# Optimization experiments

Measured on AMD Instinct MI355X. Metric: run time of the kernel, lower is better.

The kernel has to match this reference:

```python
import jax, jax.numpy as jnp
import numpy as np

# dims: batch, time, measurements, heads, value-unit, channel C = H*VU
B, T, N = 16, 256, 128
H, VU = 8, 8
C = H * VU          # 64
TU, MU = 32, 32     # temporal / spatial head dims
L = 4               # encoder layers
FE = 4              # feed-forward expansion
NEG = -1e9


def setup_inputs() -> dict:
    key = jax.random.key(0)
    ks = jax.random.split(key, 20)
    def rn(k, shape, scale=0.02):
        return jax.random.normal(k, shape, jnp.float32) * scale
    return dict(
        values=jax.random.normal(ks[0], (B, T, N), jnp.float32),
        masks=(jax.random.uniform(ks[1], (B, T, N)) < 0.85).astype(jnp.float32),
        is_train=jnp.ones((B,), jnp.float32),
        conv1_w=rn(ks[2], (C,)), conv1_b=rn(ks[3], (C,)),
        conv2_w=rn(ks[4], (C,)), conv2_b=rn(ks[5], ()),
        ln1_g=jnp.ones((L, C)), ln1_b=jnp.zeros((L, C)),
        ln2_g=jnp.ones((L, C)), ln2_b=jnp.zeros((L, C)),
        Wv_s=rn(ks[6], (L, C, C)),
        Wk_s=rn(ks[7], (L, T * C, H * MU)),
        Wq_s=rn(ks[8], (L, T * C, H * MU)),
        Wv_t=rn(ks[9], (L, C, C)),
        Wk_t=rn(ks[10], (L, N * C, H * TU)),
        Wq_t=rn(ks[11], (L, N * C, H * TU)),
        Wr=rn(ks[12], (L, 2 * C, C)), br=jnp.zeros((L, C)),
        W1=rn(ks[13], (L, C, FE * C)), b1=jnp.zeros((L, FE * C)),
        W2=rn(ks[14], (L, FE * C, C)), b2=jnp.zeros((L, C)),
    )


def layer_norm(x, g, b):
    mu = x.mean(-1, keepdims=True)
    var = ((x - mu) ** 2).mean(-1, keepdims=True)
    return (x - mu) * jax.lax.rsqrt(var + 1e-5) * g + b


def attn_core(x, Wv, Wk, Wq, hd):
    # x: [B, A, E, C]; attend over A, the extra axis E is flattened into K/Q inputs
    B_, A, E, C_ = x.shape
    v = (x @ Wv).reshape(B_, A, E, H, VU)
    flat = x.reshape(B_, A, E * C_)
    q = (flat @ Wq).reshape(B_, A, H, hd)
    k = (flat @ Wk).reshape(B_, A, H, hd)
    energy = jnp.einsum('bqhd,bkhd->bqkh', q, k)            # [B, A, A, H]
    eye = jnp.eye(A, dtype=x.dtype)[None, :, :, None]
    energy = energy * (1.0 - eye) + eye * NEG               # exclude self (imputation mask)
    attn = jax.nn.softmax(energy / jnp.sqrt(jnp.asarray(hd, x.dtype)), axis=2)
    vflat = jnp.transpose(v, (0, 1, 3, 2, 4)).reshape(B_, A, H, E * VU)
    out = jnp.einsum('bqkh,bkhd->bqhd', attn, vflat)        # [B, A, H, E*VU]
    out = out.reshape(B_, A, H, E, VU).transpose(0, 1, 3, 2, 4).reshape(B_, A, E, C_)
    return out


def reference(values, masks, is_train, conv1_w, conv1_b, conv2_w, conv2_b,
              ln1_g, ln1_b, ln2_g, ln2_b, Wv_s, Wk_s, Wq_s, Wv_t, Wk_t, Wq_t,
              Wr, br, W1, b1, W2, b2):
    # conv1 is a 1x1 conv 1->C: per-element affine lift
    x = values[..., None] * conv1_w + conv1_b               # [B, T, N, C]
    for i in range(L):
        xn = layer_norm(x, ln1_g[i], ln1_b[i])
        sp = attn_core(jnp.swapaxes(xn, 1, 2), Wv_s[i], Wk_s[i], Wq_s[i], MU)  # spatial: attend over N
        sp = jnp.swapaxes(sp, 1, 2)
        tp = attn_core(xn, Wv_t[i], Wk_t[i], Wq_t[i], TU)                      # temporal: attend over T
        x0 = jnp.concatenate([sp, tp], axis=-1)             # [B, T, N, 2C]
        x1 = x0 @ Wr[i] + br[i] + x
        h = jax.nn.relu(layer_norm(x1, ln2_g[i], ln2_b[i]) @ W1[i] + b1[i])
        x = h @ W2[i] + b2[i] + x1
    out = x @ conv2_w + conv2_b                              # conv2 1x1 C->1: [B, T, N]
    per = (masks * (out - values) ** 2).reshape(B, -1).sum(-1) / masks.reshape(B, -1).sum(-1)
    loss = jnp.sum(per * is_train) / (jnp.sum(is_train) + 1e-5)
    return out, loss
```

## Files before the change

kernel.cpp:

```cpp
#include <hip/hip_runtime.h>

typedef unsigned short u16;
typedef unsigned int u32;
typedef __attribute__((ext_vector_type(8))) short short8;
typedef __attribute__((ext_vector_type(4))) float f32x4;

#define NEGSC (-1.7677669529663689e8f)
#define INVS  (0.17677669529663687f)

__device__ __forceinline__ u16 f2bf(float f) {
  union { float f; u32 u; } x{f};
  u32 r = x.u + 0x7fffu + ((x.u >> 16) & 1u);
  return (u16)(r >> 16);
}

__global__ __launch_bounds__(256) void k_lift(const float* __restrict__ values,
    const float* __restrict__ w, const float* __restrict__ b, float* __restrict__ x) {
  int i = blockIdx.x * 256 + threadIdx.x;
  int c = i & 63;
  int r = i >> 6;
  x[i] = values[r] * w[c] + b[c];
}

__global__ __launch_bounds__(256) void k_lnb(const float* __restrict__ in, u16* __restrict__ out,
    const float* __restrict__ g, const float* __restrict__ b) {
  int row = blockIdx.x * 4 + (threadIdx.x >> 6);
  int c = threadIdx.x & 63;
  float v = in[(size_t)row * 64 + c];
  float s = v;
  #pragma unroll
  for (int o = 32; o > 0; o >>= 1) s += __shfl_xor(s, o, 64);
  float mu = s * (1.f / 64.f);
  float d = v - mu;
  float q = d * d;
  #pragma unroll
  for (int o = 32; o > 0; o >>= 1) q += __shfl_xor(q, o, 64);
  out[(size_t)row * 64 + c] = f2bf(d * rsqrtf(q * (1.f / 64.f) + 1e-5f) * g[c] + b[c]);
}

__global__ __launch_bounds__(256) void k_trb(const int4* __restrict__ in, int4* __restrict__ out) {
  int idx = blockIdx.x * 256 + threadIdx.x;
  int c8 = idx & 7;
  int r = idx >> 3;
  int t = r & 255;
  int bn = r >> 8;
  int n = bn & 127;
  int b = bn >> 7;
  out[idx] = in[(((((b << 8) + t) << 7) + n) << 3) + c8];
}

__global__ __launch_bounds__(256) void k_wcast(const float* __restrict__ in, u16* __restrict__ out,
    int K, int N) {
  __shared__ float tile[32][33];
  int k0 = blockIdx.x * 32, n0 = blockIdx.y * 32;
  int tid = threadIdx.x;
  int kr = tid >> 3, nc = (tid & 7) * 4;
  float4 v = *(const float4*)(in + (size_t)(k0 + kr) * N + n0 + nc);
  tile[kr][nc + 0] = v.x; tile[kr][nc + 1] = v.y;
  tile[kr][nc + 2] = v.z; tile[kr][nc + 3] = v.w;
  __syncthreads();
  int nr = tid >> 3, kc = (tid & 7) * 4;
  ushort4 o;
  o.x = f2bf(tile[kc + 0][nr]); o.y = f2bf(tile[kc + 1][nr]);
  o.z = f2bf(tile[kc + 2][nr]); o.w = f2bf(tile[kc + 3][nr]);
  *(ushort4*)(out + (size_t)(n0 + nr) * K + k0 + kc) = o;
}

__global__ __launch_bounds__(256) void k_zerobuf(float4* __restrict__ p) {
  p[blockIdx.x * 256 + threadIdx.x] = float4{0.f, 0.f, 0.f, 0.f};
}

template<int MODE, bool SPLITK>
__global__ __launch_bounds__(256) void k_mm(
    const u16* __restrict__ A, const u16* __restrict__ Bt, void* Cv,
    const float* __restrict__ bias, const float* res,
    int M, int N, int K, int ldb, int Ksub,
    long long sA, long long sB, int pAsh, int pEsh) {
  __shared__ int4 As4[128 * 8];
  __shared__ int4 Bs4[64 * 8];
  int tid = threadIdx.x;
  int m0 = blockIdx.x * 128, n0 = blockIdx.y * 64;
  int z = blockIdx.z;
  const u16* Ap = A;
  const u16* Bp = Bt;
  int k_beg = 0, k_end = K;
  if (SPLITK) { k_beg = z * Ksub; k_end = k_beg + Ksub; }
  else { Ap += (size_t)z * sA; Bp += (size_t)z * sB; }
  int arow = tid >> 1, aseg = tid & 1;
  int brow = tid >> 2, bq = tid & 3;
  const u16* agp = Ap + (size_t)(m0 + arow) * K + aseg * 32;
  const u16* bgp = Bp + (size_t)(n0 + brow) * ldb + bq * 16;
  int wid = tid >> 6, lane = tid & 63;
  int wr = wid >> 1, wc = wid & 1;
  int l15 = lane & 15, l4 = lane >> 4;
  f32x4 acc[4][2];
  #pragma unroll
  for (int i = 0; i < 4; i++)
    #pragma unroll
    for (int j = 0; j < 2; j++) acc[i][j] = (f32x4){0.f, 0.f, 0.f, 0.f};
  for (int k0 = k_beg; k0 < k_end; k0 += 64) {
    int4 a0 = *(const int4*)(agp + k0);
    int4 a1 = *(const int4*)(agp + k0 + 8);
    int4 a2 = *(const int4*)(agp + k0 + 16);
    int4 a3 = *(const int4*)(agp + k0 + 24);
    int4 b0 = *(const int4*)(bgp + k0);
    int4 b1 = *(const int4*)(bgp + k0 + 8);
    __syncthreads();
    int s0 = aseg * 4, sw = arow & 7;
    As4[arow * 8 + ((s0 + 0) ^ sw)] = a0;
    As4[arow * 8 + ((s0 + 1) ^ sw)] = a1;
    As4[arow * 8 + ((s0 + 2) ^ sw)] = a2;
    As4[arow * 8 + ((s0 + 3) ^ sw)] = a3;
    int swb = brow & 7;
    Bs4[brow * 8 + ((bq * 2 + 0) ^ swb)] = b0;
    Bs4[brow * 8 + ((bq * 2 + 1) ^ swb)] = b1;
    __syncthreads();
    #pragma unroll
    for (int kk = 0; kk < 2; kk++) {
      short8 af[4], bf[2];
      #pragma unroll
      for (int mi = 0; mi < 4; mi++) {
        int row = wr * 64 + mi * 16 + l15;
        af[mi] = *(const short8*)&As4[row * 8 + ((kk * 4 + l4) ^ (row & 7))];
      }
      #pragma unroll
      for (int ni = 0; ni < 2; ni++) {
        int row = wc * 32 + ni * 16 + l15;
        bf[ni] = *(const short8*)&Bs4[row * 8 + ((kk * 4 + l4) ^ (row & 7))];
      }
      #pragma unroll
      for (int mi = 0; mi < 4; mi++)
        #pragma unroll
        for (int ni = 0; ni < 2; ni++)
          acc[mi][ni] = __builtin_amdgcn_mfma_f32_16x16x32_bf16(af[mi], bf[ni], acc[mi][ni], 0, 0, 0);
    }
  }
  int b_z = z >> 3, h_z = z & 7;
  #pragma unroll
  for (int mi = 0; mi < 4; mi++) {
    #pragma unroll
    for (int ni = 0; ni < 2; ni++) {
      #pragma unroll
      for (int j = 0; j < 4; j++) {
        int row = m0 + wr * 64 + mi * 16 + l4 * 4 + j;
        int col = n0 + wc * 32 + ni * 16 + l15;
        float v = acc[mi][ni][j];
        if constexpr (MODE == 0) {
          float* C = (float*)Cv;
          if (SPLITK) {
            atomicAdd(&C[(size_t)row * N + col], v);
          } else {
            if (bias) v += bias[col];
            if (res)  v += res[(size_t)row * N + col];
            C[(size_t)row * N + col] = v;
          }
        } else if constexpr (MODE == 1) {
          u16* C = (u16*)Cv;
          v += bias[col];
          v = fmaxf(v, 0.f);
          C[(size_t)row * N + col] = f2bf(v);
        } else if constexpr (MODE == 2) {
          u16* C = (u16*)Cv;
          int bb = row >> 15;
          int a  = (row >> pEsh) & ((1 << pAsh) - 1);
          int e  = row & ((1 << pEsh) - 1);
          int h  = col >> 3, vu = col & 7;
          size_t idx = ((((size_t)(bb * 8 + h) << (pEsh + 3)) + (e << 3) + vu) << pAsh) + a;
          C[idx] = f2bf(v);
        } else if constexpr (MODE == 3) {
          u16* C = (u16*)Cv;
          C[(((size_t)(b_z * 256 + row) * 128) + (col >> 3)) * 64 + h_z * 8 + (col & 7)] = f2bf(v);
        } else if constexpr (MODE == 4) {
          u16* C = (u16*)Cv;
          C[(((size_t)(b_z * 256 + (col >> 3)) * 128) + row) * 64 + h_z * 8 + (col & 7)] = f2bf(v);
        }
      }
    }
  }
}

template<int A>
__global__ __launch_bounds__(256) void k_energy(const float* __restrict__ q,
    const float* __restrict__ k, float* __restrict__ e) {
  constexpr int SH = (A == 128) ? 7 : 8;
  int bh = blockIdx.y;
  int b = bh >> 3, h = bh & 7;
  int idx = blockIdx.x * 256 + threadIdx.x;
  int kk = idx & (A - 1);
  int qq = idx >> SH;
  const float4* qr = (const float4*)(q + (size_t)(b * A + qq) * 256 + h * 32);
  const float4* kr = (const float4*)(k + (size_t)(b * A + kk) * 256 + h * 32);
  float s = 0.f;
  #pragma unroll
  for (int d = 0; d < 8; d++) {
    float4 a = qr[d], bb = kr[d];
    s += a.x * bb.x + a.y * bb.y + a.z * bb.z + a.w * bb.w;
  }
  e[((size_t)bh * A + qq) * A + kk] = (qq == kk) ? NEGSC : s * INVS;
}

template<int A>
__global__ __launch_bounds__(256) void k_softmax_pb(const float* __restrict__ e,
    u16* __restrict__ pb) {
  int row = blockIdx.x * 4 + (threadIdx.x >> 6);
  int lane = threadIdx.x & 63;
  const float* p = e + (size_t)row * A;
  constexpr int NVv = A / 64;
  float vals[NVv];
  float mx = -3e38f;
  #pragma unroll
  for (int j = 0; j < NVv; j++) { vals[j] = p[lane + j * 64]; mx = fmaxf(mx, vals[j]); }
  #pragma unroll
  for (int o = 32; o > 0; o >>= 1) mx = fmaxf(mx, __shfl_xor(mx, o, 64));
  float s = 0.f;
  #pragma unroll
  for (int j = 0; j < NVv; j++) { vals[j] = __expf(vals[j] - mx); s += vals[j]; }
  #pragma unroll
  for (int o = 32; o > 0; o >>= 1) s += __shfl_xor(s, o, 64);
  float r = 1.f / s;
  #pragma unroll
  for (int j = 0; j < NVv; j++) pb[(size_t)row * A + lane + j * 64] = f2bf(vals[j] * r);
}

__global__ void k_zero(float* __restrict__ p) {
  if (threadIdx.x < 32) p[threadIdx.x] = 0.f;
}

__global__ __launch_bounds__(256) void k_out_loss(const float* __restrict__ x,
    const float* __restrict__ w, const float* __restrict__ cb,
    const float* __restrict__ values, const float* __restrict__ masks,
    float* __restrict__ outp, float* __restrict__ acc) {
  int wid = threadIdx.x >> 6, lane = threadIdx.x & 63;
  float lnum = 0.f, lden = 0.f;
  int base = blockIdx.x * 64;
  for (int g = 0; g < 16; g++) {
    int row = base + g * 4 + wid;
    float v = x[(size_t)row * 64 + lane] * w[lane];
    #pragma unroll
    for (int o = 32; o > 0; o >>= 1) v += __shfl_xor(v, o, 64);
    if (lane == 0) {
      float o = v + cb[0];
      outp[row] = o;
      float m = masks[row];
      float dd = o - values[row];
      lnum += m * dd * dd;
      lden += m;
    }
  }
  __shared__ float sn[4], sd[4];
  if (lane == 0) { sn[wid] = lnum; sd[wid] = lden; }
  __syncthreads();
  if (threadIdx.x == 0) {
    int b = base >> 15;
    atomicAdd(&acc[2 * b],     sn[0] + sn[1] + sn[2] + sn[3]);
    atomicAdd(&acc[2 * b + 1], sd[0] + sd[1] + sd[2] + sd[3]);
  }
}

__global__ void k_loss_final(const float* __restrict__ acc,
    const float* __restrict__ is_train, float* __restrict__ outp) {
  if (threadIdx.x == 0) {
    float s = 0.f, st = 0.f;
    for (int b = 0; b < 16; b++) {
      s  += (acc[2 * b] / acc[2 * b + 1]) * is_train[b];
      st += is_train[b];
    }
    outp[(size_t)16 * 256 * 128] = s / (st + 1e-5f);
  }
}

extern "C" void kernel_launch(void* const* d_in, const int* in_sizes, int n_in,
                              void* d_out, int out_size, void* d_ws, size_t ws_size,
                              hipStream_t stream) {
  const float* values  = (const float*)d_in[0];
  const float* masks   = (const float*)d_in[1];
  const float* is_train= (const float*)d_in[2];
  const float* conv1_w = (const float*)d_in[3];
  const float* conv1_b = (const float*)d_in[4];
  const float* conv2_w = (const float*)d_in[5];
  const float* conv2_b = (const float*)d_in[6];
  const float* ln1_g   = (const float*)d_in[7];
  const float* ln1_b   = (const float*)d_in[8];
  const float* ln2_g   = (const float*)d_in[9];
  const float* ln2_b   = (const float*)d_in[10];
  const float* Wv_s    = (const float*)d_in[11];
  const float* Wk_s    = (const float*)d_in[12];
  const float* Wq_s    = (const float*)d_in[13];
  const float* Wv_t    = (const float*)d_in[14];
  const float* Wk_t    = (const float*)d_in[15];
  const float* Wq_t    = (const float*)d_in[16];
  const float* Wr      = (const float*)d_in[17];
  const float* br      = (const float*)d_in[18];
  const float* W1      = (const float*)d_in[19];
  const float* b1      = (const float*)d_in[20];
  const float* W2      = (const float*)d_in[21];
  const float* b2      = (const float*)d_in[22];
  float* outp = (float*)d_out;

  const size_t perb = 2097152;
  char* base = (char*)d_ws;
  size_t off = 0;
  auto alloc = [&](size_t bytes) { char* p = base + off; off += (bytes + 255) & ~(size_t)255; return p; };
  float* x      = (float*)alloc(16 * perb * 4);
  u16* wq_s_b   = (u16*)alloc(4 * 4194304 * 2);
  u16* wk_s_b   = (u16*)alloc(4 * 4194304 * 2);
  u16* wq_t_b   = (u16*)alloc(4 * 2097152 * 2);
  u16* wk_t_b   = (u16*)alloc(4 * 2097152 * 2);
  u16* wv_s_b   = (u16*)alloc(4 * 4096 * 2);
  u16* wv_t_b   = (u16*)alloc(4 * 4096 * 2);
  u16* wr_b     = (u16*)alloc(4 * 8192 * 2);
  u16* w1_b     = (u16*)alloc(4 * 16384 * 2);
  u16* w2_b     = (u16*)alloc(4 * 16384 * 2);
  float* lossb  = (float*)alloc(32 * 4);
  size_t fixed = off;
  size_t perb_bytes = perb * 2 * 5 + perb * 4 + 65536 * 4 * 2 + 524288 * 4 + 524288 * 2;
  int CB = 16;
  while (CB > 1 && fixed + (size_t)CB * perb_bytes > ws_size) CB >>= 1;
  u16* xnb   = (u16*)alloc((size_t)CB * perb * 2);
  u16* xswb  = (u16*)alloc((size_t)CB * perb * 2);
  u16* x2b   = (u16*)alloc((size_t)CB * perb * 2);
  u16* hb    = (u16*)alloc((size_t)CB * perb * 2);
  u16* vhT   = (u16*)alloc((size_t)CB * perb * 2);
  float* x1  = (float*)alloc((size_t)CB * perb * 4);
  float* qb  = (float*)alloc((size_t)CB * 65536 * 4);
  float* kb  = (float*)alloc((size_t)CB * 65536 * 4);
  float* attnE = (float*)alloc((size_t)CB * 524288 * 4);
  u16* Pb    = (u16*)alloc((size_t)CB * 524288 * 2);
  u16* tpb = xnb;
  u16* spb = xswb;

  const int rowsC = CB * 32768;
  const int NC = 16 / CB;

  struct WDesc { const float* src; u16* dst; int K, N; size_t stride_in, stride_out; };
  WDesc wd[9] = {
    { Wq_s, wq_s_b, 16384, 256, 16384u * 256, 4194304 },
    { Wk_s, wk_s_b, 16384, 256, 16384u * 256, 4194304 },
    { Wq_t, wq_t_b,  8192, 256,  8192u * 256, 2097152 },
    { Wk_t, wk_t_b,  8192, 256,  8192u * 256, 2097152 },
    { Wv_s, wv_s_b,    64,  64,  4096,        4096 },
    { Wv_t, wv_t_b,    64,  64,  4096,        4096 },
    { Wr,   wr_b,     128,  64,  8192,        8192 },
    { W1,   w1_b,      64, 256, 16384,       16384 },
    { W2,   w2_b,     256,  64, 16384,       16384 },
  };
  for (int w = 0; w < 9; w++)
    for (int l = 0; l < 4; l++)
      k_wcast<<<dim3(wd[w].K / 32, wd[w].N / 32), 256, 0, stream>>>(
          wd[w].src + (size_t)l * wd[w].stride_in, wd[w].dst + (size_t)l * wd[w].stride_out,
          wd[w].K, wd[w].N);

  k_lift<<<131072, 256, 0, stream>>>(values, conv1_w, conv1_b, x);

  for (int i = 0; i < 4; i++) {
    for (int c = 0; c < NC; c++) {
      float* xc = x + (size_t)c * CB * perb;
      k_lnb<<<rowsC / 4, 256, 0, stream>>>(xc, xnb, ln1_g + i * 64, ln1_b + i * 64);
      k_trb<<<CB * 1024, 256, 0, stream>>>((const int4*)xnb, (int4*)xswb);
      k_zerobuf<<<CB * 128, 256, 0, stream>>>((float4*)qb);
      k_mm<0, true><<<dim3(CB * 2, 4, 8), 256, 0, stream>>>(
          xnb, wq_t_b + (size_t)i * 2097152, qb, nullptr, nullptr,
          CB * 256, 256, 8192, 8192, 1024, 0, 0, 0, 0);
      k_mm<0, true><<<dim3(CB * 2, 4, 8), 256, 0, stream>>>(
          xnb, wk_t_b + (size_t)i * 2097152, kb, nullptr, nullptr,
          CB * 256, 256, 8192, 8192, 1024, 0, 0, 0, 0);
      k_mm<2, false><<<dim3(rowsC / 128, 1, 1), 256, 0, stream>>>(
          xnb, wv_t_b + (size_t)i * 4096, vhT, nullptr, nullptr,
          rowsC, 64, 64, 64, 0, 0, 0, 8, 7);
      k_energy<256><<<dim3(256, CB * 8), 256, 0, stream>>>(qb, kb, attnE);
      k_softmax_pb<256><<<CB * 512, 256, 0, stream>>>(attnE, Pb);
      k_mm<3, false><<<dim3(2, 16, CB * 8), 256, 0, stream>>>(
          Pb, vhT, tpb, nullptr, nullptr,
          256, 1024, 256, 256, 0, 65536, 262144, 0, 0);
      k_zerobuf<<<CB * 128, 256, 0, stream>>>((float4*)qb);
      k_mm<0, true><<<dim3(CB, 4, 16), 256, 0, stream>>>(
          xswb, wq_s_b + (size_t)i * 4194304, qb, nullptr, nullptr,
          CB * 128, 256, 16384, 16384, 1024, 0, 0, 0, 0);
      k_mm<0, true><<<dim3(CB, 4, 16), 256, 0, stream>>>(
          xswb, wk_s_b + (size_t)i * 4194304, kb, nullptr, nullptr,
          CB * 128, 256, 16384, 16384, 1024, 0, 0, 0, 0);
      k_mm<2, false><<<dim3(rowsC / 128, 1, 1), 256, 0, stream>>>(
          xswb, wv_s_b + (size_t)i * 4096, vhT, nullptr, nullptr,
          rowsC, 64, 64, 64, 0, 0, 0, 7, 8);
      k_energy<128><<<dim3(64, CB * 8), 256, 0, stream>>>(qb, kb, attnE);
      k_softmax_pb<128><<<CB * 256, 256, 0, stream>>>(attnE, Pb);
      k_mm<4, false><<<dim3(1, 32, CB * 8), 256, 0, stream>>>(
          Pb, vhT, spb, nullptr, nullptr,
          128, 2048, 128, 128, 0, 16384, 262144, 0, 0);
      k_mm<0, false><<<dim3(rowsC / 128, 1, 1), 256, 0, stream>>>(
          spb, wr_b + (size_t)i * 8192, x1, br + i * 64, xc,
          rowsC, 64, 64, 128, 0, 0, 0, 0, 0);
      k_mm<0, false><<<dim3(rowsC / 128, 1, 1), 256, 0, stream>>>(
          tpb, wr_b + (size_t)i * 8192 + 64, x1, nullptr, x1,
          rowsC, 64, 64, 128, 0, 0, 0, 0, 0);
      k_lnb<<<rowsC / 4, 256, 0, stream>>>(x1, x2b, ln2_g + i * 64, ln2_b + i * 64);
      for (int r = 0; r < 4; r++) {
        size_t roff = (size_t)r * (rowsC / 4);
        k_mm<1, false><<<dim3(rowsC / 512, 4, 1), 256, 0, stream>>>(
            x2b + roff * 64, w1_b + (size_t)i * 16384, hb, b1 + i * 256, nullptr,
            rowsC / 4, 256, 64, 64, 0, 0, 0, 0, 0);
        k_mm<0, false><<<dim3(rowsC / 512, 1, 1), 256, 0, stream>>>(
            hb, w2_b + (size_t)i * 16384, xc + roff * 64, b2 + i * 64, x1 + roff * 64,
            rowsC / 4, 64, 256, 256, 0, 0, 0, 0, 0);
      }
    }
  }

  k_zero<<<1, 64, 0, stream>>>(lossb);
  k_out_loss<<<8192, 256, 0, stream>>>(x, conv2_w, conv2_b, values, masks, outp, lossb);
  k_loss_final<<<1, 64, 0, stream>>>(lossb, is_train, outp);
}
```

Before: 16.83 ms.

## Fuse attention stages, merge Q/K projections, use direct-to-LDS loads

Several changes land together. Layer norm now writes the transposed copy itself, replacing the separate transpose kernel. The Q and K projection weights are packed so one split-K GEMM computes both, writing partial sums that a small reduction kernel adds, instead of zeroing buffers and using atomics. Energy and softmax are fused into one kernel that stages Q and K tiles in shared memory. The two Wr GEMMs merge into one GEMM whose A operand switches source at K=64, which removes the x1 buffer so the residual updates x in place. GEMM tiles are loaded straight into LDS via global_load_lds, in exchange for extra partial-sum traffic and a dependence on that builtin being available.

Result: faster. 15.15 ms (-9.9%).

```diff
diff --git a/kernel.cpp b/kernel.cpp
--- a/kernel.cpp
+++ b/kernel.cpp
@@ -12,6 +12,17 @@
   union { float f; u32 u; } x{f};
   u32 r = x.u + 0x7fffu + ((x.u >> 16) & 1u);
   return (u16)(r >> 16);
+}
+
+__device__ __forceinline__ void gll16(const void* g, void* l) {
+#if defined(__has_builtin) && __has_builtin(__builtin_amdgcn_global_load_lds)
+  __builtin_amdgcn_global_load_lds(
+      (const __attribute__((address_space(1))) void*)g,
+      (__attribute__((address_space(3))) void*)l, 16, 0, 0);
+#else
+  int lane = threadIdx.x & 63;
+  *(int4*)((char*)l + lane * 16) = *(const int4*)((const char*)g);
+#endif
 }
 
 __global__ __launch_bounds__(256) void k_lift(const float* __restrict__ values,
@@ -23,7 +34,7 @@
 }
 
 __global__ __launch_bounds__(256) void k_lnb(const float* __restrict__ in, u16* __restrict__ out,
-    const float* __restrict__ g, const float* __restrict__ b) {
+    u16* __restrict__ out2, const float* __restrict__ g, const float* __restrict__ b) {
   int row = blockIdx.x * 4 + (threadIdx.x >> 6);
   int c = threadIdx.x & 63;
   float v = in[(size_t)row * 64 + c];
@@ -35,18 +46,14 @@
   float q = d * d;
   #pragma unroll
   for (int o = 32; o > 0; o >>= 1) q += __shfl_xor(q, o, 64);
-  out[(size_t)row * 64 + c] = f2bf(d * rsqrtf(q * (1.f / 64.f) + 1e-5f) * g[c] + b[c]);
-}
-
-__global__ __launch_bounds__(256) void k_trb(const int4* __restrict__ in, int4* __restrict__ out) {
-  int idx = blockIdx.x * 256 + threadIdx.x;
-  int c8 = idx & 7;
-  int r = idx >> 3;
-  int t = r & 255;
-  int bn = r >> 8;
-  int n = bn & 127;
-  int b = bn >> 7;
-  out[idx] = in[(((((b << 8) + t) << 7) + n) << 3) + c8];
+  u16 val = f2bf(d * rsqrtf(q * (1.f / 64.f) + 1e-5f) * g[c] + b[c]);
+  out[(size_t)row * 64 + c] = val;
+  if (out2) {
+    int rl = row & 32767;
+    int bb = row >> 15;
+    int t = rl >> 7, n = rl & 127;
+    out2[(((size_t)(bb * 128 + n)) * 256 + t) * 64 + c] = val;
+  }
 }
 
 __global__ __launch_bounds__(256) void k_wcast(const float* __restrict__ in, u16* __restrict__ out,
@@ -66,31 +73,45 @@
   *(ushort4*)(out + (size_t)(n0 + nr) * K + k0 + kc) = o;
 }
 
-__global__ __launch_bounds__(256) void k_zerobuf(float4* __restrict__ p) {
-  p[blockIdx.x * 256 + threadIdx.x] = float4{0.f, 0.f, 0.f, 0.f};
-}
-
 template<int MODE, bool SPLITK>
 __global__ __launch_bounds__(256) void k_mm(
-    const u16* __restrict__ A, const u16* __restrict__ Bt, void* Cv,
-    const float* __restrict__ bias, const float* res,
-    int M, int N, int K, int ldb, int Ksub,
+    const u16* __restrict__ A, const u16* __restrict__ A2, const u16* __restrict__ Bt,
+    void* Cv, const float* __restrict__ bias, const float* res,
+    int M, int N, int K, int lda, int ldb, int Ksub, int ksh, int Kturn,
     long long sA, long long sB, int pAsh, int pEsh) {
-  __shared__ int4 As4[128 * 8];
-  __shared__ int4 Bs4[64 * 8];
+  __shared__ __align__(16) u16 As[128 * 64];
+  __shared__ __align__(16) u16 Bs[64 * 64];
   int tid = threadIdx.x;
+  int wid = tid >> 6, lane = tid & 63;
   int m0 = blockIdx.x * 128, n0 = blockIdx.y * 64;
   int z = blockIdx.z;
   const u16* Ap = A;
   const u16* Bp = Bt;
   int k_beg = 0, k_end = K;
-  if (SPLITK) { k_beg = z * Ksub; k_end = k_beg + Ksub; }
-  else { Ap += (size_t)z * sA; Bp += (size_t)z * sB; }
-  int arow = tid >> 1, aseg = tid & 1;
-  int brow = tid >> 2, bq = tid & 3;
-  const u16* agp = Ap + (size_t)(m0 + arow) * K + aseg * 32;
-  const u16* bgp = Bp + (size_t)(n0 + brow) * ldb + bq * 16;
-  int wid = tid >> 6, lane = tid & 63;
+  if (SPLITK) {
+    int ty = z >> ksh;
+    int seg = z - (ty << ksh);
+    Bp += (size_t)ty * sB;
+    k_beg = seg * Ksub;
+    k_end = k_beg + Ksub;
+  } else {
+    Ap += (size_t)z * sA;
+    Bp += (size_t)z * sB;
+  }
+  int lrow = lane >> 3;
+  int lseg = (lane & 7) ^ lrow;
+  size_t aoff[4];
+  #pragma unroll
+  for (int i = 0; i < 4; i++) {
+    int g = wid * 4 + i;
+    aoff[i] = (size_t)(m0 + g * 8 + lrow) * lda + lseg * 8;
+  }
+  size_t boff[2];
+  #pragma unroll
+  for (int i = 0; i < 2; i++) {
+    int g = wid * 2 + i;
+    boff[i] = (size_t)(n0 + g * 8 + lrow) * ldb + lseg * 8;
+  }
   int wr = wid >> 1, wc = wid & 1;
   int l15 = lane & 15, l4 = lane >> 4;
   f32x4 acc[4][2];
@@ -99,40 +120,35 @@
     #pragma unroll
     for (int j = 0; j < 2; j++) acc[i][j] = (f32x4){0.f, 0.f, 0.f, 0.f};
   for (int k0 = k_beg; k0 < k_end; k0 += 64) {
-    int4 a0 = *(const int4*)(agp + k0);
-    int4 a1 = *(const int4*)(agp + k0 + 8);
-    int4 a2 = *(const int4*)(agp + k0 + 16);
-    int4 a3 = *(const int4*)(agp + k0 + 24);
-    int4 b0 = *(const int4*)(bgp + k0);
-    int4 b1 = *(const int4*)(bgp + k0 + 8);
+    const u16* Asrc = Ap;
+    int ka = k0;
+    if (A2 != nullptr && k0 >= Kturn) { Asrc = A2; ka = k0 - Kturn; }
     __syncthreads();
-    int s0 = aseg * 4, sw = arow & 7;
-    As4[arow * 8 + ((s0 + 0) ^ sw)] = a0;
-    As4[arow * 8 + ((s0 + 1) ^ sw)] = a1;
-    As4[arow * 8 + ((s0 + 2) ^ sw)] = a2;
-    As4[arow * 8 + ((s0 + 3) ^ sw)] = a3;
-    int swb = brow & 7;
-    Bs4[brow * 8 + ((bq * 2 + 0) ^ swb)] = b0;
-    Bs4[brow * 8 + ((bq * 2 + 1) ^ swb)] = b1;
+    #pragma unroll
+    for (int i = 0; i < 4; i++)
+      gll16(Asrc + aoff[i] + ka, (char*)As + wid * 4096 + i * 1024);
+    #pragma unroll
+    for (int i = 0; i < 2; i++)
+      gll16(Bp + boff[i] + k0, (char*)Bs + wid * 2048 + i * 1024);
     __syncthreads();
     #pragma unroll
     for (int kk = 0; kk < 2; kk++) {
-      short8 af[4], bf[2];
+      short8 af[4], bf2[2];
       #pragma unroll
       for (int mi = 0; mi < 4; mi++) {
-        int row = wr * 64 + mi * 16 + l15;
-        af[mi] = *(const short8*)&As4[row * 8 + ((kk * 4 + l4) ^ (row & 7))];
+        int r = wr * 64 + mi * 16 + l15;
+        af[mi] = *(const short8*)((const char*)As + r * 128 + (((kk * 4 + l4) ^ (r & 7)) * 16));
       }
       #pragma unroll
       for (int ni = 0; ni < 2; ni++) {
-        int row = wc * 32 + ni * 16 + l15;
-        bf[ni] = *(const short8*)&Bs4[row * 8 + ((kk * 4 + l4) ^ (row & 7))];
+        int r = wc * 32 + ni * 16 + l15;
+        bf2[ni] = *(const short8*)((const char*)Bs + r * 128 + (((kk * 4 + l4) ^ (r & 7)) * 16));
       }
       #pragma unroll
       for (int mi = 0; mi < 4; mi++)
         #pragma unroll
         for (int ni = 0; ni < 2; ni++)
-          acc[mi][ni] = __builtin_amdgcn_mfma_f32_16x16x32_bf16(af[mi], bf[ni], acc[mi][ni], 0, 0, 0);
+          acc[mi][ni] = __builtin_amdgcn_mfma_f32_16x16x32_bf16(af[mi], bf2[ni], acc[mi][ni], 0, 0, 0);
     }
   }
   int b_z = z >> 3, h_z = z & 7;
@@ -146,10 +162,11 @@
         int col = n0 + wc * 32 + ni * 16 + l15;
         float v = acc[mi][ni][j];
         if constexpr (MODE == 0) {
-          float* C = (float*)Cv;
           if (SPLITK) {
-            atomicAdd(&C[(size_t)row * N + col], v);
+            float* C = (float*)Cv + (size_t)z * M * N;
+            C[(size_t)row * N + col] = v;
           } else {
+            float* C = (float*)Cv;
             if (bias) v += bias[col];
             if (res)  v += res[(size_t)row * N + col];
             C[(size_t)row * N + col] = v;
@@ -179,47 +196,83 @@
   }
 }
 
+__global__ __launch_bounds__(256) void k_redqk(const float4* __restrict__ parts,
+    float4* __restrict__ qb, float4* __restrict__ kb, int M, int S) {
+  int i = blockIdx.x * 256 + threadIdx.x;
+  int half = M * 64;
+  int ty = (i >= half) ? 1 : 0;
+  int r = i - ty * half;
+  const float4* p = parts + (size_t)ty * S * half + r;
+  float4 s = p[0];
+  for (int sg = 1; sg < S; sg++) {
+    float4 v = p[(size_t)sg * half];
+    s.x += v.x; s.y += v.y; s.z += v.z; s.w += v.w;
+  }
+  (ty ? kb : qb)[r] = s;
+}
+
 template<int A>
-__global__ __launch_bounds__(256) void k_energy(const float* __restrict__ q,
-    const float* __restrict__ k, float* __restrict__ e) {
-  constexpr int SH = (A == 128) ? 7 : 8;
+__global__ __launch_bounds__(256) void k_esm(const float* __restrict__ qb,
+    const float* __restrict__ kb, u16* __restrict__ Pb) {
+  __shared__ float Kld[A][36];
+  __shared__ float Qld[32][36];
   int bh = blockIdx.y;
   int b = bh >> 3, h = bh & 7;
-  int idx = blockIdx.x * 256 + threadIdx.x;
-  int kk = idx & (A - 1);
-  int qq = idx >> SH;
-  const float4* qr = (const float4*)(q + (size_t)(b * A + qq) * 256 + h * 32);
-  const float4* kr = (const float4*)(k + (size_t)(b * A + kk) * 256 + h * 32);
-  float s = 0.f;
-  #pragma unroll
-  for (int d = 0; d < 8; d++) {
-    float4 a = qr[d], bb = kr[d];
-    s += a.x * bb.x + a.y * bb.y + a.z * bb.z + a.w * bb.w;
-  }
-  e[((size_t)bh * A + qq) * A + kk] = (qq == kk) ? NEGSC : s * INVS;
-}
-
-template<int A>
-__global__ __launch_bounds__(256) void k_softmax_pb(const float* __restrict__ e,
-    u16* __restrict__ pb) {
-  int row = blockIdx.x * 4 + (threadIdx.x >> 6);
-  int lane = threadIdx.x & 63;
-  const float* p = e + (size_t)row * A;
-  constexpr int NVv = A / 64;
-  float vals[NVv];
-  float mx = -3e38f;
-  #pragma unroll
-  for (int j = 0; j < NVv; j++) { vals[j] = p[lane + j * 64]; mx = fmaxf(mx, vals[j]); }
-  #pragma unroll
-  for (int o = 32; o > 0; o >>= 1) mx = fmaxf(mx, __shfl_xor(mx, o, 64));
-  float s = 0.f;
-  #pragma unroll
-  for (int j = 0; j < NVv; j++) { vals[j] = __expf(vals[j] - mx); s += vals[j]; }
-  #pragma unroll
-  for (int o = 32; o > 0; o >>= 1) s += __shfl_xor(s, o, 64);
-  float r = 1.f / s;
-  #pragma unroll
-  for (int j = 0; j < NVv; j++) pb[(size_t)row * A + lane + j * 64] = f2bf(vals[j] * r);
+  int q0 = blockIdx.x * 32;
+  int tid = threadIdx.x;
+  const float* kbase = kb + ((size_t)b * A) * 256 + h * 32;
+  #pragma unroll
+  for (int p = 0; p < A / 32; p++) {
+    int row = p * 32 + (tid >> 3);
+    int c4 = tid & 7;
+    float4 v = *(const float4*)(kbase + (size_t)row * 256 + c4 * 4);
+    *(float4*)&Kld[row][c4 * 4] = v;
+  }
+  {
+    int row = tid >> 3, c4 = tid & 7;
+    float4 v = *(const float4*)(qb + ((size_t)b * A + q0 + row) * 256 + h * 32 + c4 * 4);
+    *(float4*)&Qld[row][c4 * 4] = v;
+  }
+  __syncthreads();
+  int w = tid >> 6, lane = tid & 63;
+  constexpr int NJ = A / 64;
+  for (int rr = 0; rr < 8; rr++) {
+    int rl = w * 8 + rr;
+    int qrow = q0 + rl;
+    float qv[32];
+    #pragma unroll
+    for (int c4 = 0; c4 < 8; c4++) {
+      float4 v = *(const float4*)&Qld[rl][c4 * 4];
+      qv[c4 * 4 + 0] = v.x; qv[c4 * 4 + 1] = v.y;
+      qv[c4 * 4 + 2] = v.z; qv[c4 * 4 + 3] = v.w;
+    }
+    float vals[NJ];
+    float mx = -3e38f;
+    #pragma unroll
+    for (int jj = 0; jj < NJ; jj++) {
+      int kidx = lane + jj * 64;
+      float s = 0.f;
+      #pragma unroll
+      for (int c4 = 0; c4 < 8; c4++) {
+        float4 v = *(const float4*)&Kld[kidx][c4 * 4];
+        s += qv[c4 * 4 + 0] * v.x + qv[c4 * 4 + 1] * v.y
+           + qv[c4 * 4 + 2] * v.z + qv[c4 * 4 + 3] * v.w;
+      }
+      vals[jj] = (kidx == qrow) ? NEGSC : s * INVS;
+      mx = fmaxf(mx, vals[jj]);
+    }
+    #pragma unroll
+    for (int o = 32; o > 0; o >>= 1) mx = fmaxf(mx, __shfl_xor(mx, o, 64));
+    float ssum = 0.f;
+    #pragma unroll
+    for (int jj = 0; jj < NJ; jj++) { vals[jj] = __expf(vals[jj] - mx); ssum += vals[jj]; }
+    #pragma unroll
+    for (int o = 32; o > 0; o >>= 1) ssum += __shfl_xor(ssum, o, 64);
+    float rs = 1.f / ssum;
+    #pragma unroll
+    for (int jj = 0; jj < NJ; jj++)
+      Pb[((size_t)bh * A + qrow) * A + lane + jj * 64] = f2bf(vals[jj] * rs);
+  }
 }
 
 __global__ void k_zero(float* __restrict__ p) {
@@ -302,10 +355,8 @@
   size_t off = 0;
   auto alloc = [&](size_t bytes) { char* p = base + off; off += (bytes + 255) & ~(size_t)255; return p; };
   float* x      = (float*)alloc(16 * perb * 4);
-  u16* wq_s_b   = (u16*)alloc(4 * 4194304 * 2);
-  u16* wk_s_b   = (u16*)alloc(4 * 4194304 * 2);
-  u16* wq_t_b   = (u16*)alloc(4 * 2097152 * 2);
-  u16* wk_t_b   = (u16*)alloc(4 * 2097152 * 2);
+  u16* wqk_s_b  = (u16*)alloc((size_t)4 * 2 * 4194304 * 2);
+  u16* wqk_t_b  = (u16*)alloc((size_t)4 * 2 * 2097152 * 2);
   u16* wv_s_b   = (u16*)alloc(4 * 4096 * 2);
   u16* wv_t_b   = (u16*)alloc(4 * 4096 * 2);
   u16* wr_b     = (u16*)alloc(4 * 8192 * 2);
@@ -313,18 +364,17 @@
   u16* w2_b     = (u16*)alloc(4 * 16384 * 2);
   float* lossb  = (float*)alloc(32 * 4);
   size_t fixed = off;
-  size_t perb_bytes = perb * 2 * 5 + perb * 4 + 65536 * 4 * 2 + 524288 * 4 + 524288 * 2;
+  size_t perb_bytes = perb * 2 * 5 + 65536 * 4 * 2 + 2 * 524288 * 4 + 524288 * 2;
   int CB = 16;
-  while (CB > 1 && fixed + (size_t)CB * perb_bytes > ws_size) CB >>= 1;
+  while (CB > 1 && fixed + (size_t)CB * perb_bytes + 4096 > ws_size) CB >>= 1;
   u16* xnb   = (u16*)alloc((size_t)CB * perb * 2);
   u16* xswb  = (u16*)alloc((size_t)CB * perb * 2);
   u16* x2b   = (u16*)alloc((size_t)CB * perb * 2);
   u16* hb    = (u16*)alloc((size_t)CB * perb * 2);
   u16* vhT   = (u16*)alloc((size_t)CB * perb * 2);
-  float* x1  = (float*)alloc((size_t)CB * perb * 4);
   float* qb  = (float*)alloc((size_t)CB * 65536 * 4);
   float* kb  = (float*)alloc((size_t)CB * 65536 * 4);
-  float* attnE = (float*)alloc((size_t)CB * 524288 * 4);
+  float* parts = (float*)alloc((size_t)CB * 2 * 262144 * 4);
   u16* Pb    = (u16*)alloc((size_t)CB * 524288 * 2);
   u16* tpb = xnb;
   u16* spb = xswb;
@@ -332,22 +382,22 @@
   const int rowsC = CB * 32768;
   const int NC = 16 / CB;
 
-  struct WDesc { const float* src; u16* dst; int K, N; size_t stride_in, stride_out; };
+  struct WDesc { const float* src; u16* dst; int K, N; size_t si, so; };
   WDesc wd[9] = {
-    { Wq_s, wq_s_b, 16384, 256, 16384u * 256, 4194304 },
-    { Wk_s, wk_s_b, 16384, 256, 16384u * 256, 4194304 },
-    { Wq_t, wq_t_b,  8192, 256,  8192u * 256, 2097152 },
-    { Wk_t, wk_t_b,  8192, 256,  8192u * 256, 2097152 },
-    { Wv_s, wv_s_b,    64,  64,  4096,        4096 },
-    { Wv_t, wv_t_b,    64,  64,  4096,        4096 },
-    { Wr,   wr_b,     128,  64,  8192,        8192 },
-    { W1,   w1_b,      64, 256, 16384,       16384 },
-    { W2,   w2_b,     256,  64, 16384,       16384 },
+    { Wq_s, wqk_s_b,           16384, 256, 16384u * 256, 2u * 4194304 },
+    { Wk_s, wqk_s_b + 4194304, 16384, 256, 16384u * 256, 2u * 4194304 },
+    { Wq_t, wqk_t_b,            8192, 256,  8192u * 256, 2u * 2097152 },
+    { Wk_t, wqk_t_b + 2097152,  8192, 256,  8192u * 256, 2u * 2097152 },
+    { Wv_s, wv_s_b,    64,  64,  4096,  4096 },
+    { Wv_t, wv_t_b,    64,  64,  4096,  4096 },
+    { Wr,   wr_b,     128,  64,  8192,  8192 },
+    { W1,   w1_b,      64, 256, 16384, 16384 },
+    { W2,   w2_b,     256,  64, 16384, 16384 },
   };
   for (int w = 0; w < 9; w++)
     for (int l = 0; l < 4; l++)
       k_wcast<<<dim3(wd[w].K / 32, wd[w].N / 32), 256, 0, stream>>>(
-          wd[w].src + (size_t)l * wd[w].stride_in, wd[w].dst + (size_t)l * wd[w].stride_out,
+          wd[w].src + (size_t)l * wd[w].si, wd[w].dst + (size_t)l * wd[w].so,
           wd[w].K, wd[w].N);
 
   k_lift<<<131072, 256, 0, stream>>>(values, conv1_w, conv1_b, x);
@@ -355,53 +405,44 @@
   for (int i = 0; i < 4; i++) {
     for (int c = 0; c < NC; c++) {
       float* xc = x + (size_t)c * CB * perb;
-      k_lnb<<<rowsC / 4, 256, 0, stream>>>(xc, xnb, ln1_g + i * 64, ln1_b + i * 64);
-      k_trb<<<CB * 1024, 256, 0, stream>>>((const int4*)xnb, (int4*)xswb);
-      k_zerobuf<<<CB * 128, 256, 0, stream>>>((float4*)qb);
+      k_lnb<<<rowsC / 4, 256, 0, stream>>>(xc, xnb, xswb, ln1_g + i * 64, ln1_b + i * 64);
       k_mm<0, true><<<dim3(CB * 2, 4, 8), 256, 0, stream>>>(
-          xnb, wq_t_b + (size_t)i * 2097152, qb, nullptr, nullptr,
-          CB * 256, 256, 8192, 8192, 1024, 0, 0, 0, 0);
-      k_mm<0, true><<<dim3(CB * 2, 4, 8), 256, 0, stream>>>(
-          xnb, wk_t_b + (size_t)i * 2097152, kb, nullptr, nullptr,
-          CB * 256, 256, 8192, 8192, 1024, 0, 0, 0, 0);
+          xnb, nullptr, wqk_t_b + (size_t)i * 2 * 2097152, parts, nullptr, nullptr,
+          CB * 256, 256, 8192, 8192, 8192, 2048, 2, 0, 0, 2097152, 0, 0);
+      k_redqk<<<CB * 128, 256, 0, stream>>>((const float4*)parts, (float4*)qb, (float4*)kb,
+                                            CB * 256, 4);
       k_mm<2, false><<<dim3(rowsC / 128, 1, 1), 256, 0, stream>>>(
-          xnb, wv_t_b + (size_t)i * 4096, vhT, nullptr, nullptr,
-          rowsC, 64, 64, 64, 0, 0, 0, 8, 7);
-      k_energy<256><<<dim3(256, CB * 8), 256, 0, stream>>>(qb, kb, attnE);
-      k_softmax_pb<256><<<CB * 512, 256, 0, stream>>>(attnE, Pb);
+          xnb, nullptr, wv_t_b + (size_t)i * 4096, vhT, nullptr, nullptr,
+          rowsC, 64, 64, 64, 64, 0, 0, 0, 0, 0, 8, 7);
+      k_esm<256><<<dim3(8, CB * 8), 256, 0, stream>>>(qb, kb, Pb);
       k_mm<3, false><<<dim3(2, 16, CB * 8), 256, 0, stream>>>(
-          Pb, vhT, tpb, nullptr, nullptr,
-          256, 1024, 256, 256, 0, 65536, 262144, 0, 0);
-      k_zerobuf<<<CB * 128, 256, 0, stream>>>((float4*)qb);
+          Pb, nullptr, vhT, tpb, nullptr, nullptr,
+          256, 1024, 256, 256, 256, 0, 0, 0, 65536, 262144, 0, 0);
       k_mm<0, true><<<dim3(CB, 4, 16), 256, 0, stream>>>(
-          xswb, wq_s_b + (size_t)i * 4194304, qb, nullptr, nullptr,
-          CB * 128, 256, 16384, 16384, 1024, 0, 0, 0, 0);
-      k_mm<0, true><<<dim3(CB, 4, 16), 256, 0, stream>>>(
-          xswb, wk_s_b + (size_t)i * 4194304, kb, nullptr, nullptr,
-          CB * 128, 256, 16384, 16384, 1024, 0, 0, 0, 0);
+          xswb, nullptr, wqk_s_b + (size_t)i * 2 * 4194304, parts, nullptr, nullptr,
+          CB * 128, 256, 16384, 16384, 16384, 2048, 3, 0, 0, 4194304, 0, 0);
+      k_redqk<<<CB * 64, 256, 0, stream>>>((const float4*)parts, (float4*)qb, (float4*)kb,
+                                           CB * 128, 8);
       k_mm<2, false><<<dim3(rowsC / 128, 1, 1), 256, 0, stream>>>(
-          xswb, wv_s_b + (size_t)i * 4096, vhT, nullptr, nullptr,
-          rowsC, 64, 64, 64, 0, 0, 0, 7, 8);
-      k_energy<128><<<dim3(64, CB * 8), 256, 0, stream>>>(qb, kb, attnE);
-      k_softmax_pb<128><<<CB * 256, 256, 0, stream>>>(attnE, Pb);
+          xswb, nullptr, wv_s_b + (size_t)i * 4096, vhT, nullptr, nullptr,
+          rowsC, 64, 64, 64, 64, 0, 0, 0, 0, 0, 7, 8);
+      k_esm<128><<<dim3(4, CB * 8), 256, 0, stream>>>(qb, kb, Pb);
       k_mm<4, false><<<dim3(1, 32, CB * 8), 256, 0, stream>>>(
-          Pb, vhT, spb, nullptr, nullptr,
-          128, 2048, 128, 128, 0, 16384, 262144, 0, 0);
+          Pb, nullptr, vhT, spb, nullptr, nullptr,
+          128, 2048, 128, 128, 128, 0, 0, 0, 16384, 262144, 0, 0);
       k_mm<0, false><<<dim3(rowsC / 128, 1, 1), 256, 0, stream>>>(
-          spb, wr_b + (size_t)i * 8192, x1, br + i * 64, xc,
-          rowsC, 64, 64, 128, 0, 0, 0, 0, 0);
-      k_mm<0, false><<<dim3(rowsC / 128, 1, 1), 256, 0, stream>>>(
-          tpb, wr_b + (size_t)i * 8192 + 64, x1, nullptr, x1,
-          rowsC, 64, 64, 128, 0, 0, 0, 0, 0);
-      k_lnb<<<rowsC / 4, 256, 0, stream>>>(x1, x2b, ln2_g + i * 64, ln2_b + i * 64);
+          spb, tpb, wr_b + (size_t)i * 8192, xc, br + i * 64, xc,
+          rowsC, 64, 128, 64, 128, 0, 0, 64, 0, 0, 0, 0);
+      k_lnb<<<rowsC / 4, 256, 0, stream>>>(xc, x2b, nullptr, ln2_g + i * 64, ln2_b + i * 64);
       for (int r = 0; r < 4; r++) {
         size_t roff = (size_t)r * (rowsC / 4);
         k_mm<1, false><<<dim3(rowsC / 512, 4, 1), 256, 0, stream>>>(
-            x2b + roff * 64, w1_b + (size_t)i * 16384, hb, b1 + i * 256, nullptr,
-            rowsC / 4, 256, 64, 64, 0, 0, 0, 0, 0);
+            x2b + roff * 64, nullptr, w1_b + (size_t)i * 16384, hb, b1 + i * 256, nullptr,
+            rowsC / 4, 256, 64, 64, 64, 0, 0, 0, 0, 0, 0, 0);
         k_mm<0, false><<<dim3(rowsC / 512, 1, 1), 256, 0, stream>>>(
-            hb, w2_b + (size_t)i * 16384, xc + roff * 64, b2 + i * 64, x1 + roff * 64,
-            rowsC / 4, 64, 256, 256, 0, 0, 0, 0, 0);
+            hb, nullptr, w2_b + (size_t)i * 16384, xc + roff * 64, b2 + i * 64,
+            (const float*)(xc + roff * 64),
+            rowsC / 4, 64, 256, 256, 256, 0, 0, 0, 0, 0, 0, 0);
       }
     }
   }
```
